# Kernel tuning notes

Hardware: AMD Instinct MI355X
Metric: run time of the kernel (lower is better)

The kernel has to match this reference:

```python
import jax, jax.numpy as jnp
import numpy as np

B, T, D = 32, 1024, 1024
N, L = 77, 768
H = 8
TED = 2048  # time_embed_dim
EPS = 1e-5


def _ln(x, g, b):
    m = jnp.mean(x, axis=-1, keepdims=True)
    v = jnp.var(x, axis=-1, keepdims=True)
    return (x - m) * jax.lax.rsqrt(v + EPS) * g + b


def setup_inputs() -> dict:
    key = jax.random.key(0)
    ks = jax.random.split(key, 16)
    s = lambda fan_in: 1.0 / np.sqrt(fan_in)
    return {
        "x": jax.random.normal(ks[0], (B, T, D), jnp.float32),
        "xf": jax.random.normal(ks[1], (B, N, L), jnp.float32),
        "emb": jax.random.normal(ks[2], (B, TED), jnp.float32),
        "norm_g": jnp.ones((D,), jnp.float32),
        "norm_b": jnp.zeros((D,), jnp.float32),
        "tnorm_g": jnp.ones((L,), jnp.float32),
        "tnorm_b": jnp.zeros((L,), jnp.float32),
        "Wq": jax.random.normal(ks[3], (D, D), jnp.float32) * s(D),
        "bq": jnp.zeros((D,), jnp.float32),
        "Wk": jax.random.normal(ks[4], (L, D), jnp.float32) * s(L),
        "bk": jnp.zeros((D,), jnp.float32),
        "Wv": jax.random.normal(ks[5], (L, D), jnp.float32) * s(L),
        "bv": jnp.zeros((D,), jnp.float32),
        "emb_W": jax.random.normal(ks[6], (TED, 2 * D), jnp.float32) * s(TED),
        "emb_b": jnp.zeros((2 * D,), jnp.float32),
        "onorm_g": jnp.ones((D,), jnp.float32),
        "onorm_b": jnp.zeros((D,), jnp.float32),
        "Wo": jax.random.normal(ks[7], (D, D), jnp.float32) * s(D),
        "bo": jnp.zeros((D,), jnp.float32),
    }


def reference(x, xf, emb, norm_g, norm_b, tnorm_g, tnorm_b, Wq, bq, Wk, bk, Wv, bv,
              emb_W, emb_b, onorm_g, onorm_b, Wo, bo):
    Bc, Tc, Dc = x.shape
    Nc = xf.shape[1]
    hd = Dc // H
    # projections
    q = _ln(x, norm_g, norm_b) @ Wq + bq                      # [B,T,D]
    xfn = _ln(xf, tnorm_g, tnorm_b)                           # [B,N,L]
    k = (xfn @ Wk + bk).reshape(Bc, Nc, H, hd)                # [B,N,H,hd]
    v = (xfn @ Wv + bv).reshape(Bc, Nc, H, hd)                # [B,N,H,hd]
    q = jax.nn.softmax(q.reshape(Bc, Tc, H, hd), axis=-1)     # softmax over head_dim
    k = jax.nn.softmax(k, axis=1)                             # softmax over N (key tokens)
    # linear-attention: no TxN matrix
    attn = jnp.einsum('bnhd,bnhl->bhdl', k, v)                # [B,H,hd,hd]
    y = jnp.einsum('bthd,bhdl->bthl', q, attn).reshape(Bc, Tc, Dc)
    # StylizationBlock
    emb_out = jax.nn.silu(emb) @ emb_W + emb_b                # [B,2D]
    scale, shift = jnp.split(emb_out[:, None, :], 2, axis=2)  # [B,1,D] each
    h = _ln(y, onorm_g, onorm_b) * (1.0 + scale) + shift
    h = jax.nn.silu(h) @ Wo + bo
    return x + h
```

## Files before the change

kernel.cpp:

```cpp
#include <hip/hip_runtime.h>
#include <hip/hip_bf16.h>
#include <math.h>

namespace {

constexpr int Bc  = 32;
constexpr int Tc  = 1024;
constexpr int Dc  = 1024;
constexpr int Nt  = 77;
constexpr int Lc  = 768;
constexpr int HDc = 128;
constexpr int TEDc = 2048;
constexpr float EPSc = 1e-5f;

typedef __attribute__((ext_vector_type(8))) short bf16x8;
typedef __attribute__((ext_vector_type(8))) unsigned short u16x8;
typedef __attribute__((ext_vector_type(4))) float f32x4;

__device__ __forceinline__ float silu_f(float x) { return x / (1.f + __expf(-x)); }

__device__ __forceinline__ unsigned short f2bf(float f) {
  unsigned u = __float_as_uint(f);
  return (unsigned short)((u + 0x7fffu + ((u >> 16) & 1u)) >> 16);
}
__device__ __forceinline__ float bf2f(unsigned short h) {
  return __uint_as_float(((unsigned)h) << 16);
}

__device__ __forceinline__ void gload16(const void* g, void* l) {
  __builtin_amdgcn_global_load_lds((const __attribute__((address_space(1))) void*)g,
                                   (__attribute__((address_space(3))) void*)l, 16, 0, 0);
}

__global__ __launch_bounds__(256) void ln_bf16_kernel(
    const float* __restrict__ src, unsigned short* __restrict__ dst, int cols,
    const float* __restrict__ g, const float* __restrict__ b)
{
  const int row = blockIdx.x;
  const float* p = src + (size_t)row * cols;
  const int c = threadIdx.x * 4;
  float4 v = make_float4(0.f, 0.f, 0.f, 0.f);
  if (c < cols) v = *reinterpret_cast<const float4*>(p + c);
  float s  = v.x + v.y + v.z + v.w;
  float sq = v.x * v.x + v.y * v.y + v.z * v.z + v.w * v.w;
  __shared__ float red[2][4];
  __shared__ float mr[2];
  for (int o = 32; o > 0; o >>= 1) { s += __shfl_down(s, o); sq += __shfl_down(sq, o); }
  const int wid = threadIdx.x >> 6, lane = threadIdx.x & 63;
  if (lane == 0) { red[0][wid] = s; red[1][wid] = sq; }
  __syncthreads();
  if (threadIdx.x == 0) {
    const float S  = red[0][0] + red[0][1] + red[0][2] + red[0][3];
    const float SQ = red[1][0] + red[1][1] + red[1][2] + red[1][3];
    const float mean = S / cols;
    const float var  = SQ / cols - mean * mean;
    mr[0] = mean; mr[1] = rsqrtf(var + EPSc);
  }
  __syncthreads();
  if (c < cols) {
    const float mean = mr[0], rstd = mr[1];
    ushort4 o;
    o.x = f2bf((v.x - mean) * rstd * g[c + 0] + b[c + 0]);
    o.y = f2bf((v.y - mean) * rstd * g[c + 1] + b[c + 1]);
    o.z = f2bf((v.z - mean) * rstd * g[c + 2] + b[c + 2]);
    o.w = f2bf((v.w - mean) * rstd * g[c + 3] + b[c + 3]);
    *reinterpret_cast<ushort4*>(dst + (size_t)row * cols + c) = o;
  }
}

__global__ __launch_bounds__(256) void convT_bf16_kernel(
    const float* __restrict__ W, unsigned short* __restrict__ Wt, int K, int N)
{
  __shared__ float t[32][33];
  const int n0 = blockIdx.x * 32, k0 = blockIdx.y * 32;
  const int tx = threadIdx.x & 31, ty = threadIdx.x >> 5;
  #pragma unroll
  for (int dy = 0; dy < 32; dy += 8)
    t[ty + dy][tx] = W[(size_t)(k0 + ty + dy) * N + n0 + tx];
  __syncthreads();
  #pragma unroll
  for (int dy = 0; dy < 32; dy += 8)
    Wt[(size_t)(n0 + ty + dy) * K + k0 + tx] = f2bf(t[tx][ty + dy]);
}

__global__ __launch_bounds__(256) void convT2_bf16_kernel(
    const float* __restrict__ W0, unsigned short* __restrict__ T0,
    const float* __restrict__ W1, unsigned short* __restrict__ T1, int K, int N)
{
  __shared__ float t[32][33];
  const float* W = blockIdx.z ? W1 : W0;
  unsigned short* Wt = blockIdx.z ? T1 : T0;
  const int n0 = blockIdx.x * 32, k0 = blockIdx.y * 32;
  const int tx = threadIdx.x & 31, ty = threadIdx.x >> 5;
  #pragma unroll
  for (int dy = 0; dy < 32; dy += 8)
    t[ty + dy][tx] = W[(size_t)(k0 + ty + dy) * N + n0 + tx];
  __syncthreads();
  #pragma unroll
  for (int dy = 0; dy < 32; dy += 8)
    Wt[(size_t)(n0 + ty + dy) * K + k0 + tx] = f2bf(t[tx][ty + dy]);
}

template<int EPI>
__global__ __launch_bounds__(512) void gemm2_kernel(
    const unsigned short* __restrict__ A, const unsigned short* __restrict__ Bt,
    const float* __restrict__ bias, const float* __restrict__ bias2, int bsplit,
    void* __restrict__ Cout, int M, int K, int N, const float* __restrict__ xres)
{
  constexpr int LDSE = (EPI == 2) ? 32768 : 24576;
  __shared__ unsigned short lds[LDSE];
  const int tid = threadIdx.x, wid = tid >> 6, lane = tid & 63;
  const int ntx = N >> 7;
  int swz = blockIdx.x;
  const int nwg = gridDim.x;
  if ((nwg & 7) == 0) { const int cpx = nwg >> 3; swz = (swz & 7) * cpx + (swz >> 3); }
  const int bx = swz % ntx, by = swz / ntx;
  const int bm0 = by << 8, bn0 = bx << 7;
  const int wr = wid >> 1, wc = wid & 1, lhi = lane >> 4, llo = lane & 15;

  const int srow = lane >> 2, scol = (lane & 3) * 8;
  int ar0 = bm0 + wid * 32 + srow;      if (ar0 >= M) ar0 = M - 1;
  int ar1 = bm0 + wid * 32 + 16 + srow; if (ar1 >= M) ar1 = M - 1;
  const int br = bn0 + wid * 16 + srow;
  const unsigned short* Ag0 = A  + (size_t)ar0 * K + scol;
  const unsigned short* Ag1 = A  + (size_t)ar1 * K + scol;
  const unsigned short* Bg  = Bt + (size_t)br  * K + scol;
  const int alc0 = (wid * 2) * 512, alc1 = (wid * 2 + 1) * 512, blc = wid * 512;
  const int aoff = wr * 2048 + llo * 32 + lhi * 8;
  const int boff = wc * 2048 + llo * 32 + lhi * 8;

  f32x4 acc[4][4] = {};
  const int nt = K >> 5;

  gload16(Ag0, &lds[alc0]);
  gload16(Ag1, &lds[alc1]);
  gload16(Bg,  &lds[16384 + blc]);
  __syncthreads();

  int cur = 0;
  for (int t = 1; t < nt; ++t) {
    const int nb = cur ^ 1;
    const int k0 = t << 5;
    gload16(Ag0 + k0, &lds[nb * 8192 + alc0]);
    gload16(Ag1 + k0, &lds[nb * 8192 + alc1]);
    gload16(Bg  + k0, &lds[16384 + nb * 4096 + blc]);
    bf16x8 a_[4], b_[4];
    #pragma unroll
    for (int mi = 0; mi < 4; mi++) a_[mi] = *(const bf16x8*)(&lds[cur * 8192 + aoff + mi * 512]);
    #pragma unroll
    for (int ni = 0; ni < 4; ni++) b_[ni] = *(const bf16x8*)(&lds[16384 + cur * 4096 + boff + ni * 512]);
    #pragma unroll
    for (int mi = 0; mi < 4; mi++)
      #pragma unroll
      for (int ni = 0; ni < 4; ni++)
        acc[mi][ni] = __builtin_amdgcn_mfma_f32_16x16x32_bf16(a_[mi], b_[ni], acc[mi][ni], 0, 0, 0);
    __syncthreads();
    cur = nb;
  }
  {
    bf16x8 a_[4], b_[4];
    #pragma unroll
    for (int mi = 0; mi < 4; mi++) a_[mi] = *(const bf16x8*)(&lds[cur * 8192 + aoff + mi * 512]);
    #pragma unroll
    for (int ni = 0; ni < 4; ni++) b_[ni] = *(const bf16x8*)(&lds[16384 + cur * 4096 + boff + ni * 512]);
    #pragma unroll
    for (int mi = 0; mi < 4; mi++)
      #pragma unroll
      for (int ni = 0; ni < 4; ni++)
        acc[mi][ni] = __builtin_amdgcn_mfma_f32_16x16x32_bf16(a_[mi], b_[ni], acc[mi][ni], 0, 0, 0);
  }

  if constexpr (EPI != 2) {
    #pragma unroll
    for (int mi = 0; mi < 4; mi++) {
      #pragma unroll
      for (int ni = 0; ni < 4; ni++) {
        const int col = bn0 + wc * 64 + ni * 16 + llo;
        const float bs = (bsplit > 0 && col >= bsplit) ? bias2[col - bsplit] : bias[col];
        #pragma unroll
        for (int r = 0; r < 4; r++) {
          const int row = bm0 + wr * 64 + mi * 16 + lhi * 4 + r;
          if (row < M) {
            float v = acc[mi][ni][r] + bs;
            if (EPI == 1) v += xres[(size_t)row * N + col];
            ((float*)Cout)[(size_t)row * N + col] = v;
          }
        }
      }
    }
  } else {
    __syncthreads();
    #pragma unroll
    for (int mi = 0; mi < 4; mi++) {
      #pragma unroll
      for (int ni = 0; ni < 4; ni++) {
        const int col = wc * 64 + ni * 16 + llo;
        const float bs = bias[bn0 + col];
        #pragma unroll
        for (int r = 0; r < 4; r++) {
          const int row = wr * 64 + mi * 16 + lhi * 4 + r;
          lds[row * 128 + (col ^ ((row & 7) << 3))] = f2bf(acc[mi][ni][r] + bs);
        }
      }
    }
    __syncthreads();
    const int row = tid >> 1, cb = (tid & 1) * 64;
    const int sw = (row & 7) << 3;
    float mx = -1e30f;
    #pragma unroll
    for (int g = 0; g < 8; g++) {
      u16x8 u = *(const u16x8*)(&lds[row * 128 + ((cb + g * 8) ^ sw)]);
      #pragma unroll
      for (int j = 0; j < 8; j++) mx = fmaxf(mx, bf2f(u[j]));
    }
    mx = fmaxf(mx, __shfl_xor(mx, 1));
    float ssum = 0.f;
    #pragma unroll
    for (int g = 0; g < 8; g++) {
      unsigned short* p = &lds[row * 128 + ((cb + g * 8) ^ sw)];
      u16x8 u = *(const u16x8*)p;
      u16x8 e;
      #pragma unroll
      for (int j = 0; j < 8; j++) {
        float ev = __expf(bf2f(u[j]) - mx);
        ssum += ev;
        e[j] = f2bf(ev);
      }
      *(u16x8*)p = e;
    }
    ssum += __shfl_xor(ssum, 1);
    const float inv = 1.f / ssum;
    unsigned short* Cb = (unsigned short*)Cout;
    #pragma unroll
    for (int g = 0; g < 8; g++) {
      u16x8 u = *(const u16x8*)(&lds[row * 128 + ((cb + g * 8) ^ sw)]);
      u16x8 o;
      #pragma unroll
      for (int j = 0; j < 8; j++) o[j] = f2bf(bf2f(u[j]) * inv);
      *(u16x8*)(&Cb[(size_t)(bm0 + row) * N + bn0 + cb + g * 8]) = o;
    }
  }
}

__global__ __launch_bounds__(256) void attn_fused_kernel(
    const float* __restrict__ kv, unsigned short* __restrict__ attnT) {
  const int bh = blockIdx.x;
  const int b = bh >> 3, h = bh & 7;
  __shared__ float ks[Nt][HDc];
  __shared__ float vs[Nt][HDc];
  const float* kb = kv + (size_t)b * Nt * 2048 + h * HDc;
  const float* vb = kv + (size_t)b * Nt * 2048 + 1024 + h * HDc;
  for (int i = threadIdx.x; i < Nt * HDc; i += 256) {
    const int n = i >> 7, d = i & 127;
    ks[n][d] = kb[(size_t)n * 2048 + d];
    vs[n][d] = vb[(size_t)n * 2048 + d];
  }
  __syncthreads();
  if (threadIdx.x < HDc) {
    const int d = threadIdx.x;
    float m = -1e30f;
    for (int n = 0; n < Nt; n++) m = fmaxf(m, ks[n][d]);
    float s = 0.f;
    for (int n = 0; n < Nt; n++) { float e = __expf(ks[n][d] - m); ks[n][d] = e; s += e; }
    const float inv = 1.f / s;
    for (int n = 0; n < Nt; n++) ks[n][d] *= inv;
  }
  __syncthreads();
  const int tx = threadIdx.x & 15, ty = threadIdx.x >> 4;
  float acc[8][8] = {};
  for (int n = 0; n < Nt; n++) {
    float a[8], w[8];
    #pragma unroll
    for (int i = 0; i < 8; i++) a[i] = vs[n][ty + 16 * i];
    #pragma unroll
    for (int j = 0; j < 8; j++) w[j] = ks[n][tx + 16 * j];
    #pragma unroll
    for (int i = 0; i < 8; i++)
      #pragma unroll
      for (int j = 0; j < 8; j++)
        acc[i][j] += a[i] * w[j];
  }
  unsigned short* ab = attnT + (size_t)bh * HDc * HDc;
  #pragma unroll
  for (int i = 0; i < 8; i++)
    #pragma unroll
    for (int j = 0; j < 8; j++)
      ab[(size_t)(ty + 16 * i) * HDc + tx + 16 * j] = f2bf(acc[i][j]);
}

__global__ __launch_bounds__(256) void y_mfma_kernel(
    unsigned short* __restrict__ q, const unsigned short* __restrict__ attnT)
{
  __shared__ unsigned short lds[16384];
  const int tid = threadIdx.x, wid = tid >> 6, lane = tid & 63;
  const int bh = blockIdx.y, b = bh >> 3, h = bh & 7;
  const int bm0 = blockIdx.x << 7;
  const int wr = wid >> 1, wc = wid & 1, lhi = lane >> 4, llo = lane & 15;

  unsigned short* Abase = q + ((size_t)b * Tc) * Dc + h * HDc;
  const unsigned short* Btb = attnT + (size_t)bh * HDc * HDc;

  const int srow = lane >> 2, scol = (lane & 3) * 8;
  const int ar0 = bm0 + wid * 32 + srow, ar1 = ar0 + 16;
  const int br0 = wid * 32 + srow,       br1 = br0 + 16;
  const unsigned short* Ag0 = Abase + (size_t)ar0 * Dc + scol;
  const unsigned short* Ag1 = Abase + (size_t)ar1 * Dc + scol;
  const unsigned short* Bg0 = Btb + (size_t)br0 * HDc + scol;
  const unsigned short* Bg1 = Btb + (size_t)br1 * HDc + scol;
  const int lc0 = (wid * 2 + 0) * 512, lc1 = (wid * 2 + 1) * 512;
  const int aoff = wr * 2048 + llo * 32 + lhi * 8;
  const int boff = wc * 2048 + llo * 32 + lhi * 8;

  f32x4 acc[4][4] = {};

  gload16(Ag0, &lds[lc0]);
  gload16(Ag1, &lds[lc1]);
  gload16(Bg0, &lds[8192 + lc0]);
  gload16(Bg1, &lds[8192 + lc1]);
  __syncthreads();

  int cur = 0;
  for (int t = 1; t < 4; ++t) {
    const int nb = cur ^ 1;
    const int k0 = t << 5;
    gload16(Ag0 + k0, &lds[nb * 4096 + lc0]);
    gload16(Ag1 + k0, &lds[nb * 4096 + lc1]);
    gload16(Bg0 + k0, &lds[8192 + nb * 4096 + lc0]);
    gload16(Bg1 + k0, &lds[8192 + nb * 4096 + lc1]);
    bf16x8 a_[4], b_[4];
    #pragma unroll
    for (int mi = 0; mi < 4; mi++) a_[mi] = *(const bf16x8*)(&lds[cur * 4096 + aoff + mi * 512]);
    #pragma unroll
    for (int ni = 0; ni < 4; ni++) b_[ni] = *(const bf16x8*)(&lds[8192 + cur * 4096 + boff + ni * 512]);
    #pragma unroll
    for (int mi = 0; mi < 4; mi++)
      #pragma unroll
      for (int ni = 0; ni < 4; ni++)
        acc[mi][ni] = __builtin_amdgcn_mfma_f32_16x16x32_bf16(a_[mi], b_[ni], acc[mi][ni], 0, 0, 0);
    __syncthreads();
    cur = nb;
  }
  {
    bf16x8 a_[4], b_[4];
    #pragma unroll
    for (int mi = 0; mi < 4; mi++) a_[mi] = *(const bf16x8*)(&lds[cur * 4096 + aoff + mi * 512]);
    #pragma unroll
    for (int ni = 0; ni < 4; ni++) b_[ni] = *(const bf16x8*)(&lds[8192 + cur * 4096 + boff + ni * 512]);
    #pragma unroll
    for (int mi = 0; mi < 4; mi++)
      #pragma unroll
      for (int ni = 0; ni < 4; ni++)
        acc[mi][ni] = __builtin_amdgcn_mfma_f32_16x16x32_bf16(a_[mi], b_[ni], acc[mi][ni], 0, 0, 0);
  }

  __syncthreads();
  #pragma unroll
  for (int mi = 0; mi < 4; mi++) {
    #pragma unroll
    for (int ni = 0; ni < 4; ni++) {
      const int col = wc * 64 + ni * 16 + llo;
      #pragma unroll
      for (int r = 0; r < 4; r++) {
        const int row = wr * 64 + mi * 16 + lhi * 4 + r;
        lds[row * 128 + (col ^ ((row & 7) << 3))] = f2bf(acc[mi][ni][r]);
      }
    }
  }
  __syncthreads();
  const int row = tid >> 1, cb = (tid & 1) * 64;
  const int sw = (row & 7) << 3;
  #pragma unroll
  for (int g = 0; g < 8; g++) {
    u16x8 u = *(const u16x8*)(&lds[row * 128 + ((cb + g * 8) ^ sw)]);
    *(u16x8*)(&Abase[(size_t)(bm0 + row) * Dc + cb + g * 8]) = u;
  }
}

__global__ __launch_bounds__(256) void ln_mod_silu_bf16_kernel(
    unsigned short* __restrict__ y, const float* __restrict__ ss,
    const float* __restrict__ g, const float* __restrict__ bvec) {
  const int row = blockIdx.x;
  const int b = row >> 10;
  unsigned short* p = y + (size_t)row * Dc;
  const int c = threadIdx.x * 4;
  ushort4 u = *reinterpret_cast<const ushort4*>(p + c);
  float vv[4] = {bf2f(u.x), bf2f(u.y), bf2f(u.z), bf2f(u.w)};
  float s  = vv[0] + vv[1] + vv[2] + vv[3];
  float sq = vv[0]*vv[0] + vv[1]*vv[1] + vv[2]*vv[2] + vv[3]*vv[3];
  __shared__ float red[2][4];
  __shared__ float mr[2];
  for (int o = 32; o > 0; o >>= 1) { s += __shfl_down(s, o); sq += __shfl_down(sq, o); }
  const int wid = threadIdx.x >> 6, lane = threadIdx.x & 63;
  if (lane == 0) { red[0][wid] = s; red[1][wid] = sq; }
  __syncthreads();
  if (threadIdx.x == 0) {
    const float S  = red[0][0] + red[0][1] + red[0][2] + red[0][3];
    const float SQ = red[1][0] + red[1][1] + red[1][2] + red[1][3];
    const float mean = S / Dc;
    const float var = SQ / Dc - mean * mean;
    mr[0] = mean; mr[1] = rsqrtf(var + EPSc);
  }
  __syncthreads();
  const float mean = mr[0], rstd = mr[1];
  const float* ssb = ss + (size_t)b * 2 * Dc;
  ushort4 o;
  float t0 = (vv[0] - mean) * rstd * g[c + 0] + bvec[c + 0];
  float t1 = (vv[1] - mean) * rstd * g[c + 1] + bvec[c + 1];
  float t2 = (vv[2] - mean) * rstd * g[c + 2] + bvec[c + 2];
  float t3 = (vv[3] - mean) * rstd * g[c + 3] + bvec[c + 3];
  o.x = f2bf(silu_f(t0 * (1.f + ssb[c + 0]) + ssb[Dc + c + 0]));
  o.y = f2bf(silu_f(t1 * (1.f + ssb[c + 1]) + ssb[Dc + c + 1]));
  o.z = f2bf(silu_f(t2 * (1.f + ssb[c + 2]) + ssb[Dc + c + 2]));
  o.w = f2bf(silu_f(t3 * (1.f + ssb[c + 3]) + ssb[Dc + c + 3]));
  *reinterpret_cast<ushort4*>(p + c) = o;
}

__global__ __launch_bounds__(256) void silu_emb_kernel(
    const float* __restrict__ emb, float* __restrict__ sile) {
  const int i = (blockIdx.x * 256 + threadIdx.x) * 4;
  float4 v = *reinterpret_cast<const float4*>(emb + i);
  v.x = silu_f(v.x); v.y = silu_f(v.y); v.z = silu_f(v.z); v.w = silu_f(v.w);
  *reinterpret_cast<float4*>(sile + i) = v;
}

__global__ __launch_bounds__(256) void emb_part_kernel(
    const float* __restrict__ sile, const float* __restrict__ W,
    float* __restrict__ part) {
  const int split = blockIdx.y;
  const int n = blockIdx.x * 256 + threadIdx.x;
  const int k0 = split * 64;
  const float* se = sile + k0;
  const float* Wp = W + (size_t)k0 * (2 * Dc) + n;
  float acc[32] = {};
  for (int kk = 0; kk < 64; kk++) {
    const float w = Wp[(size_t)kk * (2 * Dc)];
    #pragma unroll
    for (int m = 0; m < 32; m++)
      acc[m] = fmaf(se[m * TEDc + kk], w, acc[m]);
  }
  float* pp = part + (size_t)split * 32 * (2 * Dc) + n;
  #pragma unroll
  for (int m = 0; m < 32; m++) pp[(size_t)m * (2 * Dc)] = acc[m];
}

__global__ __launch_bounds__(256) void emb_reduce_kernel(
    const float* __restrict__ part, const float* __restrict__ bias,
    float* __restrict__ ssb) {
  const int i = blockIdx.x * 256 + threadIdx.x;
  const int n = i & (2 * Dc - 1);
  float s = bias[n];
  #pragma unroll 8
  for (int sp = 0; sp < 32; sp++) s += part[(size_t)sp * 32 * (2 * Dc) + i];
  ssb[i] = s;
}

}

extern "C" void kernel_launch(void* const* d_in, const int* in_sizes, int n_in,
                              void* d_out, int out_size, void* d_ws, size_t ws_size,
                              hipStream_t stream) {
  const float* x       = (const float*)d_in[0];
  const float* xf      = (const float*)d_in[1];
  const float* emb     = (const float*)d_in[2];
  const float* norm_g  = (const float*)d_in[3];
  const float* norm_b  = (const float*)d_in[4];
  const float* tnorm_g = (const float*)d_in[5];
  const float* tnorm_b = (const float*)d_in[6];
  const float* Wq      = (const float*)d_in[7];
  const float* bq      = (const float*)d_in[8];
  const float* Wk      = (const float*)d_in[9];
  const float* bk      = (const float*)d_in[10];
  const float* Wv      = (const float*)d_in[11];
  const float* bv_     = (const float*)d_in[12];
  const float* emb_W   = (const float*)d_in[13];
  const float* emb_b   = (const float*)d_in[14];
  const float* onorm_g = (const float*)d_in[15];
  const float* onorm_b = (const float*)d_in[16];
  const float* Wo      = (const float*)d_in[17];
  const float* bo      = (const float*)d_in[18];
  float* out = (float*)d_out;

  char* ws = (char*)d_ws;
  unsigned short* Ab = (unsigned short*)ws;
  char* R = ws;
  unsigned short* qb   = (unsigned short*)(ws + 67108864);
  unsigned short* Wq_t = (unsigned short*)(ws + 134217728);
  unsigned short* Wk_t = (unsigned short*)(ws + 136314880);
  unsigned short* Wv_t = (unsigned short*)(ws + 137887744);
  unsigned short* Wo_t = (unsigned short*)(ws + 139460608);
  float*          ssb  = (float*)(ws + 141557760);
  float*          sile = (float*)(ws + 141819904);
  float*          part = (float*)(ws + 142082048);
  unsigned short* xfb   = (unsigned short*)(R);
  float*          kv    = (float*)(R + 3784704);
  unsigned short* attnT = (unsigned short*)(R + 23969792);

  const int Mq  = Bc * Tc;
  const int Mkv = Bc * Nt;

  ln_bf16_kernel<<<Mq, 256, 0, stream>>>(x, Ab, Dc, norm_g, norm_b);
  convT_bf16_kernel<<<dim3(Dc / 32, Dc / 32), 256, 0, stream>>>(Wq, Wq_t, Dc, Dc);
  convT2_bf16_kernel<<<dim3(Dc / 32, Lc / 32, 2), 256, 0, stream>>>(Wk, Wk_t, Wv, Wv_t, Lc, Dc);
  convT_bf16_kernel<<<dim3(Dc / 32, Dc / 32), 256, 0, stream>>>(Wo, Wo_t, Dc, Dc);

  gemm2_kernel<2><<<(Dc / 128) * (Mq / 256), 512, 0, stream>>>(
      Ab, Wq_t, bq, nullptr, 0, qb, Mq, Dc, Dc, nullptr);

  ln_bf16_kernel<<<Mkv, 256, 0, stream>>>(xf, xfb, Lc, tnorm_g, tnorm_b);
  gemm2_kernel<0><<<(2048 / 128) * ((Mkv + 255) / 256), 512, 0, stream>>>(
      xfb, Wk_t, bk, bv_, 1024, kv, Mkv, Lc, 2048, nullptr);
  attn_fused_kernel<<<Bc * 8, 256, 0, stream>>>(kv, attnT);

  silu_emb_kernel<<<(Bc * TEDc) / 1024, 256, 0, stream>>>(emb, sile);
  emb_part_kernel<<<dim3(8, 32), 256, 0, stream>>>(sile, emb_W, part);
  emb_reduce_kernel<<<(Bc * 2 * Dc) / 256, 256, 0, stream>>>(part, emb_b, ssb);

  y_mfma_kernel<<<dim3(Tc / 128, Bc * 8), 256, 0, stream>>>(qb, attnT);
  ln_mod_silu_bf16_kernel<<<Mq, 256, 0, stream>>>(qb, ssb, onorm_g, onorm_b);
  gemm2_kernel<1><<<(Dc / 128) * (Mq / 256), 512, 0, stream>>>(
      qb, Wo_t, bo, nullptr, 0, out, Mq, Dc, Dc, x);
}
```

Measured before the change: 461.0 us.

## Triple-buffer GEMM LDS pipeline with XOR swizzle and compile-time K

Restructures the bf16 MFMA GEMM main loop from double to triple buffering, with explicit vmcnt waits and raw barriers so two tiles of global->LDS loads stay in flight. It adds an XOR row swizzle on the LDS column chunks to cut bank conflicts on the fragment reads, raises priority around the MFMA block, and makes K a template parameter for full unrolling. The LDS footprint grows, and the EPI==2 epilogue's offsets into the same buffer may need to be checked against the new layout.

```diff
diff --git a/kernel.cpp b/kernel.cpp
--- a/kernel.cpp
+++ b/kernel.cpp
@@ -30,6 +30,10 @@
 __device__ __forceinline__ void gload16(const void* g, void* l) {
   __builtin_amdgcn_global_load_lds((const __attribute__((address_space(1))) void*)g,
                                    (__attribute__((address_space(3))) void*)l, 16, 0, 0);
+}
+
+__device__ __forceinline__ int rowswz(int r) {
+  return (((r >> 3) & 1) << 1) | ((r >> 1) & 1);
 }
 
 __global__ __launch_bounds__(256) void ln_bf16_kernel(
@@ -101,14 +105,14 @@
     Wt[(size_t)(n0 + ty + dy) * K + k0 + tx] = f2bf(t[tx][ty + dy]);
 }
 
-template<int EPI>
-__global__ __launch_bounds__(512) void gemm2_kernel(
+template<int EPI, int NT>
+__global__ __launch_bounds__(512, 4) void gemm2_kernel(
     const unsigned short* __restrict__ A, const unsigned short* __restrict__ Bt,
     const float* __restrict__ bias, const float* __restrict__ bias2, int bsplit,
-    void* __restrict__ Cout, int M, int K, int N, const float* __restrict__ xres)
+    void* __restrict__ Cout, int M, int N, const float* __restrict__ xres)
 {
-  constexpr int LDSE = (EPI == 2) ? 32768 : 24576;
-  __shared__ unsigned short lds[LDSE];
+  constexpr int K = NT * 32;
+  __shared__ unsigned short lds[36864];
   const int tid = threadIdx.x, wid = tid >> 6, lane = tid & 63;
   const int ntx = N >> 7;
   int swz = blockIdx.x;
@@ -118,7 +122,8 @@
   const int bm0 = by << 8, bn0 = bx << 7;
   const int wr = wid >> 1, wc = wid & 1, lhi = lane >> 4, llo = lane & 15;
 
-  const int srow = lane >> 2, scol = (lane & 3) * 8;
+  const int srow = lane >> 2;
+  const int scol = (((lane & 3) ^ rowswz(srow)) * 8);
   int ar0 = bm0 + wid * 32 + srow;      if (ar0 >= M) ar0 = M - 1;
   int ar1 = bm0 + wid * 32 + 16 + srow; if (ar1 >= M) ar1 = M - 1;
   const int br = bn0 + wid * 16 + srow;
@@ -126,48 +131,55 @@
   const unsigned short* Ag1 = A  + (size_t)ar1 * K + scol;
   const unsigned short* Bg  = Bt + (size_t)br  * K + scol;
   const int alc0 = (wid * 2) * 512, alc1 = (wid * 2 + 1) * 512, blc = wid * 512;
-  const int aoff = wr * 2048 + llo * 32 + lhi * 8;
-  const int boff = wc * 2048 + llo * 32 + lhi * 8;
+  const int rx = rowswz(llo);
+  const int aoff = wr * 2048 + llo * 32 + ((lhi ^ rx) * 8);
+  const int boff = wc * 2048 + llo * 32 + ((lhi ^ rx) * 8);
 
   f32x4 acc[4][4] = {};
-  const int nt = K >> 5;
-
-  gload16(Ag0, &lds[alc0]);
-  gload16(Ag1, &lds[alc1]);
-  gload16(Bg,  &lds[16384 + blc]);
-  __syncthreads();
-
-  int cur = 0;
-  for (int t = 1; t < nt; ++t) {
-    const int nb = cur ^ 1;
-    const int k0 = t << 5;
-    gload16(Ag0 + k0, &lds[nb * 8192 + alc0]);
-    gload16(Ag1 + k0, &lds[nb * 8192 + alc1]);
-    gload16(Bg  + k0, &lds[16384 + nb * 4096 + blc]);
-    bf16x8 a_[4], b_[4];
-    #pragma unroll
-    for (int mi = 0; mi < 4; mi++) a_[mi] = *(const bf16x8*)(&lds[cur * 8192 + aoff + mi * 512]);
-    #pragma unroll
-    for (int ni = 0; ni < 4; ni++) b_[ni] = *(const bf16x8*)(&lds[16384 + cur * 4096 + boff + ni * 512]);
-    #pragma unroll
-    for (int mi = 0; mi < 4; mi++)
-      #pragma unroll
-      for (int ni = 0; ni < 4; ni++)
-        acc[mi][ni] = __builtin_amdgcn_mfma_f32_16x16x32_bf16(a_[mi], b_[ni], acc[mi][ni], 0, 0, 0);
-    __syncthreads();
-    cur = nb;
-  }
-  {
-    bf16x8 a_[4], b_[4];
-    #pragma unroll
-    for (int mi = 0; mi < 4; mi++) a_[mi] = *(const bf16x8*)(&lds[cur * 8192 + aoff + mi * 512]);
-    #pragma unroll
-    for (int ni = 0; ni < 4; ni++) b_[ni] = *(const bf16x8*)(&lds[16384 + cur * 4096 + boff + ni * 512]);
-    #pragma unroll
-    for (int mi = 0; mi < 4; mi++)
-      #pragma unroll
-      for (int ni = 0; ni < 4; ni++)
-        acc[mi][ni] = __builtin_amdgcn_mfma_f32_16x16x32_bf16(a_[mi], b_[ni], acc[mi][ni], 0, 0, 0);
+
+  gload16(Ag0,      &lds[alc0]);
+  gload16(Ag1,      &lds[alc1]);
+  gload16(Bg,       &lds[24576 + blc]);
+  gload16(Ag0 + 32, &lds[8192 + alc0]);
+  gload16(Ag1 + 32, &lds[8192 + alc1]);
+  gload16(Bg  + 32, &lds[24576 + 4096 + blc]);
+
+  for (int t = 0; t < NT; t += 3) {
+    #pragma unroll
+    for (int j = 0; j < 3; j++) {
+      const int tt = t + j;
+      if (tt < NT) {
+        if (tt + 2 < NT) {
+          const int k2 = (tt + 2) << 5;
+          constexpr int PB0 = 2, PB1 = 0, PB2 = 1;
+          const int pb = (j == 0) ? PB0 : (j == 1) ? PB1 : PB2;
+          gload16(Ag0 + k2, &lds[pb * 8192 + alc0]);
+          gload16(Ag1 + k2, &lds[pb * 8192 + alc1]);
+          gload16(Bg  + k2, &lds[24576 + pb * 4096 + blc]);
+          asm volatile("s_waitcnt vmcnt(6)" ::: "memory");
+        } else if (tt + 1 < NT) {
+          asm volatile("s_waitcnt vmcnt(3)" ::: "memory");
+        } else {
+          asm volatile("s_waitcnt vmcnt(0)" ::: "memory");
+        }
+        __builtin_amdgcn_s_barrier();
+        bf16x8 a_[4], b_[4];
+        #pragma unroll
+        for (int mi = 0; mi < 4; mi++)
+          a_[mi] = *(const bf16x8*)(&lds[j * 8192 + aoff + mi * 512]);
+        #pragma unroll
+        for (int ni = 0; ni < 4; ni++)
+          b_[ni] = *(const bf16x8*)(&lds[24576 + j * 4096 + boff + ni * 512]);
+        __builtin_amdgcn_s_setprio(1);
+        #pragma unroll
+        for (int mi = 0; mi < 4; mi++)
+          #pragma unroll
+          for (int ni = 0; ni < 4; ni++)
+            acc[mi][ni] = __builtin_amdgcn_mfma_f32_16x16x32_bf16(a_[mi], b_[ni], acc[mi][ni], 0, 0, 0);
+        __builtin_amdgcn_s_setprio(0);
+        __builtin_amdgcn_s_barrier();
+      }
+    }
   }
 
   if constexpr (EPI != 2) {
@@ -503,12 +515,12 @@
   convT2_bf16_kernel<<<dim3(Dc / 32, Lc / 32, 2), 256, 0, stream>>>(Wk, Wk_t, Wv, Wv_t, Lc, Dc);
   convT_bf16_kernel<<<dim3(Dc / 32, Dc / 32), 256, 0, stream>>>(Wo, Wo_t, Dc, Dc);
 
-  gemm2_kernel<2><<<(Dc / 128) * (Mq / 256), 512, 0, stream>>>(
-      Ab, Wq_t, bq, nullptr, 0, qb, Mq, Dc, Dc, nullptr);
+  gemm2_kernel<2, 32><<<(Dc / 128) * (Mq / 256), 512, 0, stream>>>(
+      Ab, Wq_t, bq, nullptr, 0, qb, Mq, Dc, nullptr);
 
   ln_bf16_kernel<<<Mkv, 256, 0, stream>>>(xf, xfb, Lc, tnorm_g, tnorm_b);
-  gemm2_kernel<0><<<(2048 / 128) * ((Mkv + 255) / 256), 512, 0, stream>>>(
-      xfb, Wk_t, bk, bv_, 1024, kv, Mkv, Lc, 2048, nullptr);
+  gemm2_kernel<0, 24><<<(2048 / 128) * ((Mkv + 255) / 256), 512, 0, stream>>>(
+      xfb, Wk_t, bk, bv_, 1024, kv, Mkv, 2048, nullptr);
   attn_fused_kernel<<<Bc * 8, 256, 0, stream>>>(kv, attnT);
 
   silu_emb_kernel<<<(Bc * TEDc) / 1024, 256, 0, stream>>>(emb, sile);
@@ -517,6 +529,6 @@
 
   y_mfma_kernel<<<dim3(Tc / 128, Bc * 8), 256, 0, stream>>>(qb, attnT);
   ln_mod_silu_bf16_kernel<<<Mq, 256, 0, stream>>>(qb, ssb, onorm_g, onorm_b);
-  gemm2_kernel<1><<<(Dc / 128) * (Mq / 256), 512, 0, stream>>>(
-      qb, Wo_t, bo, nullptr, 0, out, Mq, Dc, Dc, x);
-}
+  gemm2_kernel<1, 32><<<(Dc / 128) * (Mq / 256), 512, 0, stream>>>(
+      qb, Wo_t, bo, nullptr, 0, out, Mq, Dc, x);
+}
```

Result: no change. 467.4 us (+1.4%).
